# Kernel tuning notes

Measured on AMD Instinct MI355X. Metric: run time of the kernel, lower is better.

The kernel has to match this reference:

```python
import jax, jax.numpy as jnp
import numpy as np

N_NODES = 50000
N_EDGES = 625000
FEAT = 128
NEG_SLOPE = 0.2  # dgl GATConv default leaky_relu slope


def setup_inputs() -> dict:
    key = jax.random.key(0)
    ks = jax.random.split(key, 16)
    x = jax.random.normal(ks[0], (N_NODES, FEAT), dtype=jnp.float32)
    src = jax.random.randint(ks[1], (N_EDGES,), 0, N_NODES, dtype=jnp.int32)
    dst = jax.random.randint(ks[2], (N_EDGES,), 0, N_NODES, dtype=jnp.int32)
    s = 1.0 / np.sqrt(FEAT)
    d = {"x": x, "src": src, "dst": dst}
    for i in range(3):
        d[f"W{i+1}"] = jax.random.normal(ks[3 + 4 * i], (FEAT, FEAT), dtype=jnp.float32) * s
        d[f"al{i+1}"] = jax.random.normal(ks[4 + 4 * i], (FEAT,), dtype=jnp.float32) * s
        d[f"ar{i+1}"] = jax.random.normal(ks[5 + 4 * i], (FEAT,), dtype=jnp.float32) * s
        d[f"b{i+1}"] = jnp.zeros((FEAT,), dtype=jnp.float32)
    return d


def gat_layer(h_in, src, dst, W, al, ar, b):
    # dgl GATConv, num_heads=1: fc -> edge attention -> edge_softmax -> scatter
    h = h_in @ W                                   # [N, F]
    el = h @ al                                    # [N]
    er = h @ ar                                    # [N]
    e = jax.nn.leaky_relu(el[src] + er[dst], NEG_SLOPE)   # [E]
    # numerically stable edge softmax, grouped by destination node
    m = jax.ops.segment_max(e, dst, num_segments=N_NODES)  # [N]
    ex = jnp.exp(e - m[dst])
    denom = jax.ops.segment_sum(ex, dst, num_segments=N_NODES)
    alpha = ex / denom[dst]                        # [E]
    out = jax.ops.segment_sum(alpha[:, None] * h[src], dst, num_segments=N_NODES)
    return out + b


def reference(x, src, dst, W1, al1, ar1, b1, W2, al2, ar2, b2, W3, al3, ar3, b3):
    h = gat_layer(x, src, dst, W1, al1, ar1, b1)
    h = jax.nn.relu(h)
    h = gat_layer(h, src, dst, W2, al2, ar2, b2)
    h = jax.nn.relu(h)
    h = gat_layer(h, src, dst, W3, al3, ar3, b3)
    return h
```

## Files before the change

kernel.cpp:

```cpp
#include <hip/hip_runtime.h>
#include <hip/hip_fp16.h>

#define N_NODES 50000
#define N_EDGES 625000
#define FEAT 128
#define NEG_SLOPE 0.2f
#define NB_SCAN 196

typedef __attribute__((ext_vector_type(8))) short bf16x8;
typedef __attribute__((ext_vector_type(4))) float f32x4;

__device__ __forceinline__ unsigned short f2bf(float f) {
  unsigned u = __float_as_uint(f);
  u += 0x7fffu + ((u >> 16) & 1u);
  return (unsigned short)(u >> 16);
}
__device__ __forceinline__ float bf2f(unsigned short s) {
  return __uint_as_float(((unsigned)s) << 16);
}


__global__ __launch_bounds__(256) void hist_kernel(const int* __restrict__ dst,
                                                   int* __restrict__ cnt) {
  int e = blockIdx.x * 256 + threadIdx.x;
  if (e < N_EDGES) atomicAdd(&cnt[dst[e]], 1);
}

__global__ __launch_bounds__(256) void scan_part_kernel(const int* __restrict__ cnt,
                                                        int* __restrict__ part) {
  __shared__ int s[256];
  int i = blockIdx.x * 256 + threadIdx.x;
  s[threadIdx.x] = (i < N_NODES) ? cnt[i] : 0;
  __syncthreads();
  for (int o = 128; o > 0; o >>= 1) {
    if (threadIdx.x < o) s[threadIdx.x] += s[threadIdx.x + o];
    __syncthreads();
  }
  if (threadIdx.x == 0) part[blockIdx.x] = s[0];
}

__global__ __launch_bounds__(256) void scan_top_kernel(int* __restrict__ part,
                                                       int* __restrict__ offs) {
  __shared__ int s[256];
  int tid = threadIdx.x;
  int v = (tid < NB_SCAN) ? part[tid] : 0;
  s[tid] = v;
  __syncthreads();
  for (int o = 1; o < 256; o <<= 1) {
    int t = (tid >= o) ? s[tid - o] : 0;
    __syncthreads();
    s[tid] += t;
    __syncthreads();
  }
  if (tid < NB_SCAN) part[tid] = s[tid] - v;
  if (tid == 255) offs[N_NODES] = s[255];
}

__global__ __launch_bounds__(256) void scan_down_kernel(int* __restrict__ cnt,
                                                        const int* __restrict__ part,
                                                        int* __restrict__ offs) {
  __shared__ int s[256];
  int tid = threadIdx.x;
  int i = blockIdx.x * 256 + tid;
  int v = (i < N_NODES) ? cnt[i] : 0;
  s[tid] = v;
  __syncthreads();
  for (int o = 1; o < 256; o <<= 1) {
    int t = (tid >= o) ? s[tid - o] : 0;
    __syncthreads();
    s[tid] += t;
    __syncthreads();
  }
  if (i < N_NODES) {
    int excl = s[tid] - v + part[blockIdx.x];
    offs[i] = excl;
    cnt[i] = excl;
  }
}

__global__ __launch_bounds__(256) void fill_kernel(const int* __restrict__ src,
                                                   const int* __restrict__ dst,
                                                   int* __restrict__ cursor,
                                                   int* __restrict__ ssrc) {
  int e = blockIdx.x * 256 + threadIdx.x;
  if (e < N_EDGES) {
    int pos = atomicAdd(&cursor[dst[e]], 1);
    ssrc[pos] = src[e];
  }
}


__global__ __launch_bounds__(256) void prep_w_kernel(
    const float* __restrict__ W0, const float* __restrict__ W1, const float* __restrict__ W2,
    unsigned short* __restrict__ wfhi, unsigned short* __restrict__ wflo) {
  int idx = blockIdx.x * 256 + threadIdx.x;
  if (idx >= 3 * FEAT * FEAT) return;
  int l = idx >> 14, rem = idx & 16383;
  int e = rem & 7, lane = (rem >> 3) & 63, kb = (rem >> 9) & 3, ct = rem >> 11;
  int col = ct * 16 + (lane & 15);
  int k   = kb * 32 + (lane >> 4) * 8 + e;
  const float* W = (l == 0) ? W0 : ((l == 1) ? W1 : W2);
  float v = W[k * FEAT + col];
  unsigned short hi = f2bf(v);
  wfhi[idx] = hi;
  wflo[idx] = f2bf(v - bf2f(hi));
}


__global__ __launch_bounds__(256) void gemm_mfma_kernel(
    const float* __restrict__ in,
    const unsigned short* __restrict__ wfhi, const unsigned short* __restrict__ wflo,
    const float* __restrict__ al, const float* __restrict__ ar,
    __half* __restrict__ h, float* __restrict__ el, float* __restrict__ er,
    int applyRelu)
{
  const int tid = threadIdx.x;
  const int wave = tid >> 6, lane = tid & 63;
  const int lrow = lane & 15, lkb = lane >> 4;
  const int arow_i = blockIdx.x * 64 + wave * 16 + lrow;
  const bool avalid = arow_i < N_NODES;

  bf16x8 ahi[4], alo[4];
  const float* arow = in + (size_t)arow_i * FEAT;
#pragma unroll
  for (int kb = 0; kb < 4; ++kb) {
    float a[8];
    if (avalid) {
      float4 v0 = *(const float4*)(arow + kb * 32 + lkb * 8);
      float4 v1 = *(const float4*)(arow + kb * 32 + lkb * 8 + 4);
      a[0] = v0.x; a[1] = v0.y; a[2] = v0.z; a[3] = v0.w;
      a[4] = v1.x; a[5] = v1.y; a[6] = v1.z; a[7] = v1.w;
    } else {
#pragma unroll
      for (int e = 0; e < 8; ++e) a[e] = 0.f;
    }
    if (applyRelu) {
#pragma unroll
      for (int e = 0; e < 8; ++e) a[e] = fmaxf(a[e], 0.f);
    }
#pragma unroll
    for (int e = 0; e < 8; ++e) {
      unsigned short hb = f2bf(a[e]);
      ahi[kb][e] = (short)hb;
      alo[kb][e] = (short)f2bf(a[e] - bf2f(hb));
    }
  }

  f32x4 acc[8];
#pragma unroll
  for (int ct = 0; ct < 8; ++ct)
#pragma unroll
    for (int r = 0; r < 4; ++r) acc[ct][r] = 0.f;

#pragma unroll
  for (int ct = 0; ct < 8; ++ct) {
#pragma unroll
    for (int kb = 0; kb < 4; ++kb) {
      const int off = (ct * 4 + kb) * 512 + lane * 8;
      bf16x8 bhi = *(const bf16x8*)(wfhi + off);
      bf16x8 blo = *(const bf16x8*)(wflo + off);
      acc[ct] = __builtin_amdgcn_mfma_f32_16x16x32_bf16(ahi[kb], bhi, acc[ct], 0, 0, 0);
      acc[ct] = __builtin_amdgcn_mfma_f32_16x16x32_bf16(ahi[kb], blo, acc[ct], 0, 0, 0);
      acc[ct] = __builtin_amdgcn_mfma_f32_16x16x32_bf16(alo[kb], bhi, acc[ct], 0, 0, 0);
    }
  }

  float alv[8], arv[8];
#pragma unroll
  for (int ct = 0; ct < 8; ++ct) { alv[ct] = al[ct * 16 + lrow]; arv[ct] = ar[ct * 16 + lrow]; }

  const int obase = blockIdx.x * 64 + wave * 16 + lkb * 4;
#pragma unroll
  for (int r = 0; r < 4; ++r) {
    const int grow = obase + r;
    const bool gv = grow < N_NODES;
    float pel = 0.f, per_ = 0.f;
    if (gv) {
      __half* hrow = h + (size_t)grow * FEAT;
#pragma unroll
      for (int ct = 0; ct < 8; ++ct) {
        float v = acc[ct][r];
        hrow[ct * 16 + lrow] = __float2half_rn(v);
        pel  = fmaf(v, alv[ct], pel);
        per_ = fmaf(v, arv[ct], per_);
      }
    }
#pragma unroll
    for (int mask = 8; mask >= 1; mask >>= 1) {
      pel  += __shfl_xor(pel, mask);
      per_ += __shfl_xor(per_, mask);
    }
    if (gv && lrow == 0) { el[grow] = pel; er[grow] = per_; }
  }
}


__global__ __launch_bounds__(256) void agg_kernel(
    const __half* __restrict__ h, const float* __restrict__ el,
    const float* __restrict__ er, const int* __restrict__ offs,
    const int* __restrict__ ssrc, const float* __restrict__ bias,
    float* __restrict__ out)
{
  const int wid = (blockIdx.x * 256 + threadIdx.x) >> 6;
  const int lane = threadIdx.x & 63;
  if (wid >= N_NODES) return;

  const int beg = offs[wid], end = offs[wid + 1];
  const float erd = er[wid];
  const __half2* __restrict__ hh = (const __half2*)h;

  float2 acc = make_float2(0.f, 0.f);
  float denom = 0.f;
  float m = -1e30f;

  for (int base = beg; base < end; base += 64) {
    const int n = min(64, end - base);

    int s = 0;
    float e = -1e30f;
    if (lane < n) {
      s = ssrc[base + lane];
      float t = el[s] + erd;
      e = t > 0.f ? t : NEG_SLOPE * t;
    }

    float cm = e;
#pragma unroll
    for (int mask = 32; mask > 0; mask >>= 1) cm = fmaxf(cm, __shfl_xor(cm, mask));
    if (cm > m) {
      float scale = __expf(m - cm);
      acc.x *= scale; acc.y *= scale; denom *= scale;
      m = cm;
    }

    float ex = (lane < n) ? __expf(e - m) : 0.f;
    float dsum = ex;
#pragma unroll
    for (int mask = 32; mask > 0; mask >>= 1) dsum += __shfl_xor(dsum, mask);
    denom += dsum;

    int j = 0;
    for (; j + 4 <= n; j += 4) {
      int   s0 = __shfl(s, j),      s1 = __shfl(s, j + 1);
      int   s2 = __shfl(s, j + 2),  s3 = __shfl(s, j + 3);
      float e0 = __shfl(ex, j),     e1 = __shfl(ex, j + 1);
      float e2 = __shfl(ex, j + 2), e3 = __shfl(ex, j + 3);
      float2 v0 = __half22float2(hh[(s0 << 6) + lane]);
      float2 v1 = __half22float2(hh[(s1 << 6) + lane]);
      float2 v2 = __half22float2(hh[(s2 << 6) + lane]);
      float2 v3 = __half22float2(hh[(s3 << 6) + lane]);
      acc.x = fmaf(e0, v0.x, acc.x); acc.y = fmaf(e0, v0.y, acc.y);
      acc.x = fmaf(e1, v1.x, acc.x); acc.y = fmaf(e1, v1.y, acc.y);
      acc.x = fmaf(e2, v2.x, acc.x); acc.y = fmaf(e2, v2.y, acc.y);
      acc.x = fmaf(e3, v3.x, acc.x); acc.y = fmaf(e3, v3.y, acc.y);
    }
    for (; j < n; ++j) {
      int   sj = __shfl(s, j);
      float ej = __shfl(ex, j);
      float2 v = __half22float2(hh[(sj << 6) + lane]);
      acc.x = fmaf(ej, v.x, acc.x); acc.y = fmaf(ej, v.y, acc.y);
    }
  }

  float inv = denom > 0.f ? 1.f / denom : 0.f;
  float2 bv = ((const float2*)bias)[lane];
  float2 o = make_float2(fmaf(acc.x, inv, bv.x), fmaf(acc.y, inv, bv.y));
  ((float2*)out)[(wid << 6) + lane] = o;
}


extern "C" void kernel_launch(void* const* d_in, const int* in_sizes, int n_in,
                              void* d_out, int out_size, void* d_ws, size_t ws_size,
                              hipStream_t stream) {
  const float* x  = (const float*)d_in[0];
  const int* src  = (const int*)d_in[1];
  const int* dst  = (const int*)d_in[2];
  const float* W[3]  = {(const float*)d_in[3],  (const float*)d_in[7],  (const float*)d_in[11]};
  const float* al[3] = {(const float*)d_in[4],  (const float*)d_in[8],  (const float*)d_in[12]};
  const float* ar[3] = {(const float*)d_in[5],  (const float*)d_in[9],  (const float*)d_in[13]};
  const float* b[3]  = {(const float*)d_in[6],  (const float*)d_in[10], (const float*)d_in[14]};

  __half* hH  = (__half*)d_ws;
  float*  el  = (float*)(hH + 6400000);
  float*  er  = el + 50016;
  int*    cnt = (int*)(er + 50016);
  int*    offs = cnt + 50016;
  int*    part = offs + 50016;
  int*    ssrc = part + 256;
  unsigned short* wfhi = (unsigned short*)(ssrc + 625000);
  unsigned short* wflo = wfhi + 3 * FEAT * FEAT;

  prep_w_kernel<<<(3 * FEAT * FEAT + 255) / 256, 256, 0, stream>>>(W[0], W[1], W[2], wfhi, wflo);
  hipMemsetAsync(cnt, 0, N_NODES * sizeof(int), stream);
  hist_kernel<<<(N_EDGES + 255) / 256, 256, 0, stream>>>(dst, cnt);
  scan_part_kernel<<<NB_SCAN, 256, 0, stream>>>(cnt, part);
  scan_top_kernel<<<1, 256, 0, stream>>>(part, offs);
  scan_down_kernel<<<NB_SCAN, 256, 0, stream>>>(cnt, part, offs);
  fill_kernel<<<(N_EDGES + 255) / 256, 256, 0, stream>>>(src, dst, cnt, ssrc);

  const int gemm_grid = (N_NODES + 63) / 64;
  const int agg_grid  = (N_NODES + 3) / 4;
  float* outf = (float*)d_out;

  for (int l = 0; l < 3; ++l) {
    const float* lin = (l == 0) ? x : outf;
    gemm_mfma_kernel<<<gemm_grid, 256, 0, stream>>>(
        lin, wfhi + l * FEAT * FEAT, wflo + l * FEAT * FEAT,
        al[l], ar[l], hH, el, er, l > 0 ? 1 : 0);
    agg_kernel<<<agg_grid, 256, 0, stream>>>(hH, el, er, offs, ssrc, b[l], outf);
  }
}
```

Measured before the change: 236.7 us.

## Stage GEMM output through LDS and gather 16-byte rows in aggregation

The GEMM epilogue now writes its fp16 results into a shared-memory tile and then stores whole rows to global memory with coalesced 16-byte writes, replacing the scattered 2-byte stores. The aggregation kernel splits each wave into four 16-lane groups. Each group gathers a full 256-byte neighbor row using uint4 loads, so four edges are in flight per iteration instead of one per wave-wide 4-byte load. Partial sums are combined across groups with cross-lane shuffles at the end. This adds an LDS round-trip and a barrier in the GEMM and more accumulator registers in the aggregation kernel.

```diff
diff --git a/kernel.cpp b/kernel.cpp
--- a/kernel.cpp
+++ b/kernel.cpp
@@ -114,6 +114,7 @@
     __half* __restrict__ h, float* __restrict__ el, float* __restrict__ er,
     int applyRelu)
 {
+  __shared__ __half tile[64][132];
   const int tid = threadIdx.x;
   const int wave = tid >> 6, lane = tid & 63;
   const int lrow = lane & 15, lkb = lane >> 4;
@@ -169,28 +170,37 @@
 #pragma unroll
   for (int ct = 0; ct < 8; ++ct) { alv[ct] = al[ct * 16 + lrow]; arv[ct] = ar[ct * 16 + lrow]; }
 
-  const int obase = blockIdx.x * 64 + wave * 16 + lkb * 4;
+  const int lrow0 = wave * 16 + lkb * 4;
 #pragma unroll
   for (int r = 0; r < 4; ++r) {
-    const int grow = obase + r;
-    const bool gv = grow < N_NODES;
     float pel = 0.f, per_ = 0.f;
-    if (gv) {
-      __half* hrow = h + (size_t)grow * FEAT;
-#pragma unroll
-      for (int ct = 0; ct < 8; ++ct) {
-        float v = acc[ct][r];
-        hrow[ct * 16 + lrow] = __float2half_rn(v);
-        pel  = fmaf(v, alv[ct], pel);
-        per_ = fmaf(v, arv[ct], per_);
-      }
+#pragma unroll
+    for (int ct = 0; ct < 8; ++ct) {
+      float v = acc[ct][r];
+      tile[lrow0 + r][ct * 16 + lrow] = __float2half_rn(v);
+      pel  = fmaf(v, alv[ct], pel);
+      per_ = fmaf(v, arv[ct], per_);
     }
 #pragma unroll
     for (int mask = 8; mask >= 1; mask >>= 1) {
       pel  += __shfl_xor(pel, mask);
       per_ += __shfl_xor(per_, mask);
     }
-    if (gv && lrow == 0) { el[grow] = pel; er[grow] = per_; }
+    int grow = blockIdx.x * 64 + lrow0 + r;
+    if (grow < N_NODES && lrow == 0) { el[grow] = pel; er[grow] = per_; }
+  }
+  __syncthreads();
+
+  const int row0g = blockIdx.x * 64;
+#pragma unroll
+  for (int it = 0; it < 4; ++it) {
+    int idx = it * 256 + tid;
+    int row = idx >> 4, c16 = idx & 15;
+    int grow = row0g + row;
+    if (grow < N_NODES) {
+      uint4 v = *(const uint4*)&tile[row][c16 * 8];
+      *((uint4*)(h + (size_t)grow * FEAT) + c16) = v;
+    }
   }
 }
 
@@ -204,14 +214,17 @@
   const int wid = (blockIdx.x * 256 + threadIdx.x) >> 6;
   const int lane = threadIdx.x & 63;
   if (wid >= N_NODES) return;
+  const int qg = lane >> 4;
+  const int ql = lane & 15;
 
   const int beg = offs[wid], end = offs[wid + 1];
   const float erd = er[wid];
-  const __half2* __restrict__ hh = (const __half2*)h;
-
-  float2 acc = make_float2(0.f, 0.f);
-  float denom = 0.f;
-  float m = -1e30f;
+  const unsigned short* __restrict__ hu = (const unsigned short*)h;
+
+  float acc[8];
+#pragma unroll
+  for (int f = 0; f < 8; ++f) acc[f] = 0.f;
+  float denom = 0.f, m = -1e30f;
 
   for (int base = beg; base < end; base += 64) {
     const int n = min(64, end - base);
@@ -228,44 +241,59 @@
 #pragma unroll
     for (int mask = 32; mask > 0; mask >>= 1) cm = fmaxf(cm, __shfl_xor(cm, mask));
     if (cm > m) {
-      float scale = __expf(m - cm);
-      acc.x *= scale; acc.y *= scale; denom *= scale;
+      float sc = __expf(m - cm);
+#pragma unroll
+      for (int f = 0; f < 8; ++f) acc[f] *= sc;
+      denom *= sc;
       m = cm;
     }
 
     float ex = (lane < n) ? __expf(e - m) : 0.f;
-    float dsum = ex;
-#pragma unroll
-    for (int mask = 32; mask > 0; mask >>= 1) dsum += __shfl_xor(dsum, mask);
-    denom += dsum;
-
-    int j = 0;
-    for (; j + 4 <= n; j += 4) {
-      int   s0 = __shfl(s, j),      s1 = __shfl(s, j + 1);
-      int   s2 = __shfl(s, j + 2),  s3 = __shfl(s, j + 3);
-      float e0 = __shfl(ex, j),     e1 = __shfl(ex, j + 1);
-      float e2 = __shfl(ex, j + 2), e3 = __shfl(ex, j + 3);
-      float2 v0 = __half22float2(hh[(s0 << 6) + lane]);
-      float2 v1 = __half22float2(hh[(s1 << 6) + lane]);
-      float2 v2 = __half22float2(hh[(s2 << 6) + lane]);
-      float2 v3 = __half22float2(hh[(s3 << 6) + lane]);
-      acc.x = fmaf(e0, v0.x, acc.x); acc.y = fmaf(e0, v0.y, acc.y);
-      acc.x = fmaf(e1, v1.x, acc.x); acc.y = fmaf(e1, v1.y, acc.y);
-      acc.x = fmaf(e2, v2.x, acc.x); acc.y = fmaf(e2, v2.y, acc.y);
-      acc.x = fmaf(e3, v3.x, acc.x); acc.y = fmaf(e3, v3.y, acc.y);
-    }
-    for (; j < n; ++j) {
-      int   sj = __shfl(s, j);
-      float ej = __shfl(ex, j);
-      float2 v = __half22float2(hh[(sj << 6) + lane]);
-      acc.x = fmaf(ej, v.x, acc.x); acc.y = fmaf(ej, v.y, acc.y);
-    }
+    float ds = ex;
+#pragma unroll
+    for (int mask = 32; mask > 0; mask >>= 1) ds += __shfl_xor(ds, mask);
+    denom += ds;
+
+    for (int g = 0; g < n; g += 16) {
+      uint4 raw[4];
+      float w[4];
+#pragma unroll
+      for (int l = 0; l < 4; ++l) {
+        int j = g + l * 4 + qg;
+        int sj = __shfl(s, j);
+        w[l] = __shfl(ex, j);
+        raw[l] = *(const uint4*)(hu + (((size_t)sj) << 7) + (ql << 3));
+      }
+#pragma unroll
+      for (int l = 0; l < 4; ++l) {
+        float2 f0 = __half22float2(__builtin_bit_cast(__half2, raw[l].x));
+        float2 f1 = __half22float2(__builtin_bit_cast(__half2, raw[l].y));
+        float2 f2 = __half22float2(__builtin_bit_cast(__half2, raw[l].z));
+        float2 f3 = __half22float2(__builtin_bit_cast(__half2, raw[l].w));
+        acc[0] = fmaf(w[l], f0.x, acc[0]); acc[1] = fmaf(w[l], f0.y, acc[1]);
+        acc[2] = fmaf(w[l], f1.x, acc[2]); acc[3] = fmaf(w[l], f1.y, acc[3]);
+        acc[4] = fmaf(w[l], f2.x, acc[4]); acc[5] = fmaf(w[l], f2.y, acc[5]);
+        acc[6] = fmaf(w[l], f3.x, acc[6]); acc[7] = fmaf(w[l], f3.y, acc[7]);
+      }
+    }
+  }
+
+#pragma unroll
+  for (int f = 0; f < 8; ++f) {
+    acc[f] += __shfl_xor(acc[f], 16);
+    acc[f] += __shfl_xor(acc[f], 32);
   }
 
   float inv = denom > 0.f ? 1.f / denom : 0.f;
-  float2 bv = ((const float2*)bias)[lane];
-  float2 o = make_float2(fmaf(acc.x, inv, bv.x), fmaf(acc.y, inv, bv.y));
-  ((float2*)out)[(wid << 6) + lane] = o;
+  if (qg < 2) {
+    float4 bv = ((const float4*)bias)[ql * 2 + qg];
+    float4 o;
+    o.x = fmaf(acc[qg * 4 + 0], inv, bv.x);
+    o.y = fmaf(acc[qg * 4 + 1], inv, bv.y);
+    o.z = fmaf(acc[qg * 4 + 2], inv, bv.z);
+    o.w = fmaf(acc[qg * 4 + 3], inv, bv.w);
+    ((float4*)out)[((size_t)wid << 5) + ql * 2 + qg] = o;
+  }
 }
 
 
```

New measurement: 238.5 us. No clear change (+0.8%).
